# Kernel tuning notes

Hardware: AMD Instinct MI355X
Metric: run time of the kernel (lower is better)

The kernel has to match this reference:

```python
import jax, jax.numpy as jnp
import numpy as np

B, L, H = 32, 512, 1024
Q = 128
VA_H = 256

def setup_inputs() -> dict:
    key = jax.random.key(0)
    ks = jax.random.split(key, 12)
    hidden_states = jax.random.normal(ks[0], (B, L, H), dtype=jnp.float32)
    # Build valid inclusive spans: start in [2, L-16), length in [0, 8)
    asp_s = jax.random.randint(ks[1], (B, Q), 2, L - 16)
    asp_e = asp_s + jax.random.randint(ks[2], (B, Q), 0, 8)
    opi_s = jax.random.randint(ks[3], (B, Q), 2, L - 16)
    opi_e = opi_s + jax.random.randint(ks[4], (B, Q), 0, 8)
    null = jax.random.uniform(ks[5], (B, Q)) < 0.1
    asp_s = jnp.where(null, 0, asp_s)
    quad_spans = jnp.stack([asp_s, asp_e, opi_s, opi_e], axis=-1).astype(jnp.int64)
    quad_mask = (jax.random.uniform(ks[6], (B, Q)) > 0.3).astype(jnp.float32)
    # MLP params (torch Linear: y = x @ W.T + b), kaiming-ish scale
    def lin(k, out_d, in_d):
        return jax.random.normal(k, (out_d, in_d), dtype=jnp.float32) / np.sqrt(in_d)
    W1 = lin(ks[7], VA_H, 3 * H); b1 = jnp.zeros((VA_H,), jnp.float32)
    W2 = lin(ks[8], VA_H // 2, VA_H); b2 = jnp.zeros((VA_H // 2,), jnp.float32)
    W3 = lin(ks[9], 2, VA_H // 2); b3 = jnp.zeros((2,), jnp.float32)
    return {"hidden_states": hidden_states, "quad_spans": quad_spans,
            "quad_mask": quad_mask, "W1": W1, "b1": b1, "W2": W2, "b2": b2,
            "W3": W3, "b3": b3}

def _pool_spans(hidden_states, s, e):
    # hidden_states: [B,L,H]; s,e: [B,Q] inclusive indices
    pos = jnp.arange(hidden_states.shape[1])  # [L]
    valid = (s >= 2) & (e >= s)               # [B,Q]
    m = (pos[None, None, :] >= s[..., None]) & (pos[None, None, :] <= e[..., None])
    m = (m & valid[..., None]).astype(hidden_states.dtype)  # [B,Q,L]
    cnt = jnp.maximum(m.sum(-1, keepdims=True), 1.0)        # [B,Q,1]
    mean = jnp.einsum('bql,blh->bqh', m, hidden_states) / cnt
    sep = hidden_states[:, 1:2, :]                           # [B,1,H] fallback
    return jnp.where(valid[..., None], mean, sep)

def reference(hidden_states, quad_spans, quad_mask, W1, b1, W2, b2, W3, b3):
    h_asp = _pool_spans(hidden_states, quad_spans[..., 0], quad_spans[..., 1])
    h_opi = _pool_spans(hidden_states, quad_spans[..., 2], quad_spans[..., 3])
    h_pair = jnp.concatenate([h_asp, h_opi, h_asp * h_opi], axis=-1)  # [B,Q,3H]
    x = jax.nn.gelu(h_pair @ W1.T + b1, approximate=False)  # torch GELU = erf
    x = jax.nn.gelu(x @ W2.T + b2, approximate=False)
    va = jax.nn.sigmoid(x @ W3.T + b3) * 8.0 + 1.0          # [B,Q,2] in [1,9]
    # Invalid pairs stay zero, matching the torch loop's skipped entries
    return va * (quad_mask >= 0.5).astype(va.dtype)[..., None]
```

## Files before the change

kernel.cpp:

```cpp
#include <hip/hip_runtime.h>
#include <hip/hip_bf16.h>
#include <math.h>

typedef __bf16 bf16x8 __attribute__((ext_vector_type(8)));
typedef float f32x4 __attribute__((ext_vector_type(4)));

__device__ __forceinline__ unsigned short f2bf(float x) {
    union { float f; unsigned int u; } v; v.f = x;
    unsigned int r = v.u + 0x7fffu + ((v.u >> 16) & 1u);
    return (unsigned short)(r >> 16);
}
__device__ __forceinline__ float gelu_exact(float v) {
    return 0.5f * v * (1.0f + erff(v * 0.70710678118654752f));
}

__global__ __launch_bounds__(256) void prep_kernel(const float* __restrict__ hs,
                                                   const int* __restrict__ spans,
                                                   const float* __restrict__ W1,
                                                   unsigned short* __restrict__ hp,
                                                   unsigned short* __restrict__ w1b,
                                                   float* __restrict__ xacc1) {
    const int blk = blockIdx.x;
    const int tid = threadIdx.x;

    if (blk >= 4096) {
        if (blk < 4864) {
            const int i = (blk - 4096) * 256 + tid;
            float4 f = ((const float4*)W1)[i];
            ushort4 u;
            u.x = f2bf(f.x); u.y = f2bf(f.y); u.z = f2bf(f.z); u.w = f2bf(f.w);
            ((ushort4*)w1b)[i] = u;
        } else {
            const int i = (blk - 4864) * 256 + tid;
            ((float4*)xacc1)[i] = make_float4(0.f, 0.f, 0.f, 0.f);
        }
        return;
    }

    const int pair = blk;
    const int b = pair >> 7;

    const bool is64 = (spans[1] == 0);
    int s_a, e_a, s_o, e_o;
    if (is64) {
        s_a = spans[(pair * 4 + 0) * 2]; e_a = spans[(pair * 4 + 1) * 2];
        s_o = spans[(pair * 4 + 2) * 2]; e_o = spans[(pair * 4 + 3) * 2];
    } else {
        s_a = spans[pair * 4 + 0]; e_a = spans[pair * 4 + 1];
        s_o = spans[pair * 4 + 2]; e_o = spans[pair * 4 + 3];
    }

    const float4* base = (const float4*)hs + (size_t)b * 512 * 256;

    float4 A, O;
    if (s_a >= 2 && e_a >= s_a) {
        float sx = 0.f, sy = 0.f, sz = 0.f, sw = 0.f;
        for (int t = s_a; t <= e_a; ++t) {
            float4 v = base[t * 256 + tid];
            sx += v.x; sy += v.y; sz += v.z; sw += v.w;
        }
        float inv = 1.0f / (float)(e_a - s_a + 1);
        A.x = sx * inv; A.y = sy * inv; A.z = sz * inv; A.w = sw * inv;
    } else {
        A = base[256 + tid];
    }
    if (s_o >= 2 && e_o >= s_o) {
        float sx = 0.f, sy = 0.f, sz = 0.f, sw = 0.f;
        for (int t = s_o; t <= e_o; ++t) {
            float4 v = base[t * 256 + tid];
            sx += v.x; sy += v.y; sz += v.z; sw += v.w;
        }
        float inv = 1.0f / (float)(e_o - s_o + 1);
        O.x = sx * inv; O.y = sy * inv; O.z = sz * inv; O.w = sw * inv;
    } else {
        O = base[256 + tid];
    }

    unsigned short* row = hp + (size_t)pair * 3072;
    const int d = tid * 4;
    ushort4 pa, po, pp;
    pa.x = f2bf(A.x); pa.y = f2bf(A.y); pa.z = f2bf(A.z); pa.w = f2bf(A.w);
    po.x = f2bf(O.x); po.y = f2bf(O.y); po.z = f2bf(O.z); po.w = f2bf(O.w);
    pp.x = f2bf(A.x * O.x); pp.y = f2bf(A.y * O.y);
    pp.z = f2bf(A.z * O.z); pp.w = f2bf(A.w * O.w);
    *(ushort4*)(row + d) = pa;
    *(ushort4*)(row + 1024 + d) = po;
    *(ushort4*)(row + 2048 + d) = pp;
}

__global__ __launch_bounds__(256, 2) void gemm1_mfma(const unsigned short* __restrict__ A,
                                                     const unsigned short* __restrict__ Bw,
                                                     float* __restrict__ xacc) {
    __shared__ __align__(16) unsigned short As[128 * 64];
    __shared__ __align__(16) unsigned short Bs[128 * 64];

    const int tid = threadIdx.x;
    const int lane = tid & 63;
    const int wid = tid >> 6;
    const int quad = lane >> 4;
    const int l16 = lane & 15;
    const int wM = (wid >> 1) * 64;
    const int wN = (wid & 1) * 64;
    const int m0 = blockIdx.x * 128;
    const int n0 = blockIdx.y * 128;
    const int kb = blockIdx.z * 384;

    const int srow = tid >> 3;
    const int lchunk = (tid & 7) ^ (srow & 7);
    const unsigned short* Abase = A + (size_t)(m0 + srow) * 3072 + kb + lchunk * 8;
    const unsigned short* Bbase = Bw + (size_t)(n0 + srow) * 3072 + kb + lchunk * 8;

    int aoff[4][2], boff[4][2];
#pragma unroll
    for (int mi = 0; mi < 4; ++mi) {
#pragma unroll
        for (int h = 0; h < 2; ++h) {
            int row = wM + mi * 16 + l16;
            int pc = (h * 4 + quad) ^ (row & 7);
            aoff[mi][h] = row * 64 + pc * 8;
            row = wN + mi * 16 + l16;
            pc = (h * 4 + quad) ^ (row & 7);
            boff[mi][h] = row * 64 + pc * 8;
        }
    }

    f32x4 acc[4][4] = {};

#pragma unroll
    for (int it = 0; it < 6; ++it) {
        const int kadv = it * 64;
#pragma unroll
        for (int j = 0; j < 4; ++j) {
            __builtin_amdgcn_global_load_lds(
                (const __attribute__((address_space(1))) void*)(Abase + (size_t)j * 32 * 3072 + kadv),
                (__attribute__((address_space(3))) void*)(&As[(j * 256 + tid) * 8]),
                16, 0, 0);
            __builtin_amdgcn_global_load_lds(
                (const __attribute__((address_space(1))) void*)(Bbase + (size_t)j * 32 * 3072 + kadv),
                (__attribute__((address_space(3))) void*)(&Bs[(j * 256 + tid) * 8]),
                16, 0, 0);
        }
        __syncthreads();
#pragma unroll
        for (int h = 0; h < 2; ++h) {
            bf16x8 af[4], bfr[4];
#pragma unroll
            for (int mi = 0; mi < 4; ++mi) af[mi] = *(const bf16x8*)&As[aoff[mi][h]];
#pragma unroll
            for (int ni = 0; ni < 4; ++ni) bfr[ni] = *(const bf16x8*)&Bs[boff[ni][h]];
#pragma unroll
            for (int mi = 0; mi < 4; ++mi)
#pragma unroll
                for (int ni = 0; ni < 4; ++ni)
                    acc[mi][ni] = __builtin_amdgcn_mfma_f32_16x16x32_bf16(
                        af[mi], bfr[ni], acc[mi][ni], 0, 0, 0);
        }
        __syncthreads();
    }

#pragma unroll
    for (int mi = 0; mi < 4; ++mi) {
#pragma unroll
        for (int ni = 0; ni < 4; ++ni) {
            const int n = n0 + wN + ni * 16 + l16;
#pragma unroll
            for (int rr = 0; rr < 4; ++rr) {
                const int m = m0 + wM + mi * 16 + quad * 4 + rr;
                unsafeAtomicAdd(&xacc[(size_t)m * 256 + n], acc[mi][ni][rr]);
            }
        }
    }
}

__global__ __launch_bounds__(256) void gelu_bias(const float* __restrict__ xacc,
                                                 const float* __restrict__ bias,
                                                 unsigned short* __restrict__ xout,
                                                 int total4, int ncols4) {
    for (int i = blockIdx.x * blockDim.x + threadIdx.x; i < total4;
         i += gridDim.x * blockDim.x) {
        float4 v = ((const float4*)xacc)[i];
        float4 bv = ((const float4*)bias)[i & (ncols4 - 1)];
        ushort4 u;
        u.x = f2bf(gelu_exact(v.x + bv.x));
        u.y = f2bf(gelu_exact(v.y + bv.y));
        u.z = f2bf(gelu_exact(v.z + bv.z));
        u.w = f2bf(gelu_exact(v.w + bv.w));
        ((ushort4*)xout)[i] = u;
    }
}

__global__ __launch_bounds__(256) void mlp2_head(const unsigned short* __restrict__ x1,
                                                 const float* __restrict__ W2f,
                                                 const float* __restrict__ b2,
                                                 const float* __restrict__ W3,
                                                 const float* __restrict__ b3,
                                                 const float* __restrict__ mask,
                                                 float* __restrict__ out) {
    __shared__ __align__(16) unsigned short Xs[32][72];
    __shared__ __align__(16) unsigned short Ws[128][72];
    __shared__ float X2[32][132];

    const int tid = threadIdx.x;
    const int lane = tid & 63;
    const int wid = tid >> 6;
    const int wM = (wid >> 1) * 16;
    const int wN = (wid & 1) * 64;
    const int quad = lane >> 4;
    const int l16 = lane & 15;
    const int m0 = blockIdx.x * 32;

    f32x4 acc[4] = {};

    for (int k0 = 0; k0 < 256; k0 += 64) {
        {
            const int r = tid >> 3, c = (tid & 7) * 8;
            *(uint4*)&Xs[r][c] = *(const uint4*)(x1 + (size_t)(m0 + r) * 256 + k0 + c);
        }
#pragma unroll
        for (int p = 0; p < 4; ++p) {
            const int v = tid + p * 256;
            const int r = v >> 3, c = (v & 7) * 8;
            const float* src = W2f + (size_t)r * 256 + k0 + c;
            float4 f0 = *(const float4*)src;
            float4 f1 = *(const float4*)(src + 4);
            ushort4 u;
            u.x = f2bf(f0.x); u.y = f2bf(f0.y); u.z = f2bf(f0.z); u.w = f2bf(f0.w);
            *(ushort4*)&Ws[r][c] = u;
            u.x = f2bf(f1.x); u.y = f2bf(f1.y); u.z = f2bf(f1.z); u.w = f2bf(f1.w);
            *(ushort4*)&Ws[r][c + 4] = u;
        }
        __syncthreads();
#pragma unroll
        for (int kk = 0; kk < 64; kk += 32) {
            bf16x8 a = *(const bf16x8*)&Xs[wM + l16][kk + quad * 8];
#pragma unroll
            for (int ni = 0; ni < 4; ++ni) {
                bf16x8 b = *(const bf16x8*)&Ws[wN + ni * 16 + l16][kk + quad * 8];
                acc[ni] = __builtin_amdgcn_mfma_f32_16x16x32_bf16(a, b, acc[ni], 0, 0, 0);
            }
        }
        __syncthreads();
    }

#pragma unroll
    for (int ni = 0; ni < 4; ++ni) {
        const int n = wN + ni * 16 + l16;
        const float bn = b2[n];
#pragma unroll
        for (int rr = 0; rr < 4; ++rr) {
            const int m = wM + quad * 4 + rr;
            X2[m][n] = gelu_exact(acc[ni][rr] + bn);
        }
    }
    __syncthreads();

    const int p = tid >> 3;
    const int cc = (tid & 7) * 16;
    float a0 = 0.f, a1 = 0.f;
#pragma unroll
    for (int j = 0; j < 16; ++j) {
        const float xv = X2[p][cc + j];
        a0 += xv * W3[cc + j];
        a1 += xv * W3[128 + cc + j];
    }
    a0 += __shfl_xor(a0, 1); a0 += __shfl_xor(a0, 2); a0 += __shfl_xor(a0, 4);
    a1 += __shfl_xor(a1, 1); a1 += __shfl_xor(a1, 2); a1 += __shfl_xor(a1, 4);
    if ((tid & 7) == 0) {
        const int pair = m0 + p;
        const float mk = (mask[pair] >= 0.5f) ? 1.0f : 0.0f;
        out[pair * 2 + 0] = ((1.0f / (1.0f + expf(-(a0 + b3[0])))) * 8.0f + 1.0f) * mk;
        out[pair * 2 + 1] = ((1.0f / (1.0f + expf(-(a1 + b3[1])))) * 8.0f + 1.0f) * mk;
    }
}

extern "C" void kernel_launch(void* const* d_in, const int* in_sizes, int n_in,
                              void* d_out, int out_size, void* d_ws, size_t ws_size,
                              hipStream_t stream) {
    const float* hs   = (const float*)d_in[0];
    const int*   spans= (const int*)d_in[1];
    const float* mask = (const float*)d_in[2];
    const float* W1   = (const float*)d_in[3];
    const float* b1   = (const float*)d_in[4];
    const float* W2   = (const float*)d_in[5];
    const float* b2   = (const float*)d_in[6];
    const float* W3   = (const float*)d_in[7];
    const float* b3   = (const float*)d_in[8];
    float* out = (float*)d_out;

    unsigned short* hp    = (unsigned short*)d_ws;
    float*          xacc1 = (float*)((char*)d_ws + 25165824);
    unsigned short* w1b   = (unsigned short*)((char*)d_ws + 29360128);
    unsigned short* x1    = (unsigned short*)d_ws;

    prep_kernel<<<dim3(5888), dim3(256), 0, stream>>>(hs, spans, W1, hp, w1b, xacc1);
    gemm1_mfma<<<dim3(32, 2, 8), dim3(256), 0, stream>>>(hp, w1b, xacc1);
    gelu_bias<<<dim3(512), dim3(256), 0, stream>>>(xacc1, b1, x1, 4096 * 256 / 4, 64);
    mlp2_head<<<dim3(128), dim3(256), 0, stream>>>(x1, W2, b2, W3, b3, mask, out);
}
```

Before: 166.4 us.

## Fuse GELU, second MLP layer and head into GEMM1 via last-block counter

The separate gelu_bias and mlp2_head kernels are removed. Each GEMM1 block increments a per-row-tile atomic counter after its split-K atomic adds, and the 16th (last) block for a 128-row tile reads the accumulated fp32 results, applies bias and GELU, and runs the 256->128 MLP with MFMA plus the 2-output head. This saves two kernel launches and the bf16 intermediate round-trip, at the cost of serialising the tail work onto 32 last-arriving blocks. It also relies on correct fences and atomics for cross-block visibility.

```diff
diff --git a/kernel.cpp b/kernel.cpp
--- a/kernel.cpp
+++ b/kernel.cpp
@@ -9,6 +9,10 @@
     union { float f; unsigned int u; } v; v.f = x;
     unsigned int r = v.u + 0x7fffu + ((v.u >> 16) & 1u);
     return (unsigned short)(r >> 16);
+}
+__device__ __forceinline__ float bf2f(unsigned short h) {
+    union { unsigned int u; float f; } v; v.u = ((unsigned int)h) << 16;
+    return v.f;
 }
 __device__ __forceinline__ float gelu_exact(float v) {
     return 0.5f * v * (1.0f + erff(v * 0.70710678118654752f));
@@ -19,12 +23,14 @@
                                                    const float* __restrict__ W1,
                                                    unsigned short* __restrict__ hp,
                                                    unsigned short* __restrict__ w1b,
-                                                   float* __restrict__ xacc1) {
+                                                   float* __restrict__ xacc1,
+                                                   int* __restrict__ cnt) {
     const int blk = blockIdx.x;
     const int tid = threadIdx.x;
 
     if (blk >= 4096) {
         if (blk < 4864) {
+            if (blk == 4096 && tid < 32) cnt[tid] = 0;
             const int i = (blk - 4096) * 256 + tid;
             float4 f = ((const float4*)W1)[i];
             ushort4 u;
@@ -88,11 +94,21 @@
     *(ushort4*)(row + 2048 + d) = pp;
 }
 
-__global__ __launch_bounds__(256, 2) void gemm1_mfma(const unsigned short* __restrict__ A,
+__global__ __launch_bounds__(256, 2) void gemm_fused(const unsigned short* __restrict__ A,
                                                      const unsigned short* __restrict__ Bw,
-                                                     float* __restrict__ xacc) {
-    __shared__ __align__(16) unsigned short As[128 * 64];
-    __shared__ __align__(16) unsigned short Bs[128 * 64];
+                                                     float* __restrict__ xacc,
+                                                     const float* __restrict__ b1,
+                                                     const float* __restrict__ W2f,
+                                                     const float* __restrict__ b2,
+                                                     const float* __restrict__ W3,
+                                                     const float* __restrict__ b3,
+                                                     const float* __restrict__ mask,
+                                                     float* __restrict__ out,
+                                                     int* __restrict__ cnt) {
+    __shared__ __align__(16) unsigned short smem[17408];
+    __shared__ int s_last;
+    unsigned short* As = smem;
+    unsigned short* Bs = smem + 8192;
 
     const int tid = threadIdx.x;
     const int lane = tid & 63;
@@ -124,21 +140,98 @@
         }
     }
 
-    f32x4 acc[4][4] = {};
-
-#pragma unroll
-    for (int it = 0; it < 6; ++it) {
-        const int kadv = it * 64;
-#pragma unroll
-        for (int j = 0; j < 4; ++j) {
-            __builtin_amdgcn_global_load_lds(
-                (const __attribute__((address_space(1))) void*)(Abase + (size_t)j * 32 * 3072 + kadv),
-                (__attribute__((address_space(3))) void*)(&As[(j * 256 + tid) * 8]),
-                16, 0, 0);
-            __builtin_amdgcn_global_load_lds(
-                (const __attribute__((address_space(1))) void*)(Bbase + (size_t)j * 32 * 3072 + kadv),
-                (__attribute__((address_space(3))) void*)(&Bs[(j * 256 + tid) * 8]),
-                16, 0, 0);
+    {
+        f32x4 acc[4][4] = {};
+#pragma unroll
+        for (int it = 0; it < 6; ++it) {
+            const int kadv = it * 64;
+#pragma unroll
+            for (int j = 0; j < 4; ++j) {
+                __builtin_amdgcn_global_load_lds(
+                    (const __attribute__((address_space(1))) void*)(Abase + (size_t)j * 32 * 3072 + kadv),
+                    (__attribute__((address_space(3))) void*)(&As[(j * 256 + tid) * 8]),
+                    16, 0, 0);
+                __builtin_amdgcn_global_load_lds(
+                    (const __attribute__((address_space(1))) void*)(Bbase + (size_t)j * 32 * 3072 + kadv),
+                    (__attribute__((address_space(3))) void*)(&Bs[(j * 256 + tid) * 8]),
+                    16, 0, 0);
+            }
+            __syncthreads();
+#pragma unroll
+            for (int h = 0; h < 2; ++h) {
+                bf16x8 af[4], bfr[4];
+#pragma unroll
+                for (int mi = 0; mi < 4; ++mi) af[mi] = *(const bf16x8*)&As[aoff[mi][h]];
+#pragma unroll
+                for (int ni = 0; ni < 4; ++ni) bfr[ni] = *(const bf16x8*)&Bs[boff[ni][h]];
+#pragma unroll
+                for (int mi = 0; mi < 4; ++mi)
+#pragma unroll
+                    for (int ni = 0; ni < 4; ++ni)
+                        acc[mi][ni] = __builtin_amdgcn_mfma_f32_16x16x32_bf16(
+                            af[mi], bfr[ni], acc[mi][ni], 0, 0, 0);
+            }
+            __syncthreads();
+        }
+
+#pragma unroll
+        for (int mi = 0; mi < 4; ++mi) {
+#pragma unroll
+            for (int ni = 0; ni < 4; ++ni) {
+                const int n = n0 + wN + ni * 16 + l16;
+#pragma unroll
+                for (int rr = 0; rr < 4; ++rr) {
+                    const int m = m0 + wM + mi * 16 + quad * 4 + rr;
+                    unsafeAtomicAdd(&xacc[(size_t)m * 256 + n], acc[mi][ni][rr]);
+                }
+            }
+        }
+    }
+
+    __syncthreads();
+    if (tid == 0) {
+        __threadfence();
+        int old = __hip_atomic_fetch_add(&cnt[blockIdx.x], 1,
+                                         __ATOMIC_ACQ_REL, __HIP_MEMORY_SCOPE_AGENT);
+        s_last = (old == 15) ? 1 : 0;
+    }
+    __syncthreads();
+    if (!s_last) return;
+
+    f32x4 acc2[4][4] = {};
+#pragma unroll
+    for (int kc = 0; kc < 4; ++kc) {
+#pragma unroll
+        for (int s4 = 0; s4 < 4; ++s4) {
+            const int s = s4 * 256 + tid;
+            const int row = s >> 3;
+            const int pc = s & 7;
+            const int lc = pc ^ (row & 7);
+            const int col = kc * 64 + lc * 8;
+            const float* xsrc = xacc + (size_t)(m0 + row) * 256 + col;
+            float v[8];
+#pragma unroll
+            for (int j = 0; j < 8; ++j)
+                v[j] = __hip_atomic_load(xsrc + j, __ATOMIC_RELAXED,
+                                         __HIP_MEMORY_SCOPE_AGENT);
+            ushort4 u0, u1;
+            u0.x = f2bf(gelu_exact(v[0] + b1[col + 0]));
+            u0.y = f2bf(gelu_exact(v[1] + b1[col + 1]));
+            u0.z = f2bf(gelu_exact(v[2] + b1[col + 2]));
+            u0.w = f2bf(gelu_exact(v[3] + b1[col + 3]));
+            u1.x = f2bf(gelu_exact(v[4] + b1[col + 4]));
+            u1.y = f2bf(gelu_exact(v[5] + b1[col + 5]));
+            u1.z = f2bf(gelu_exact(v[6] + b1[col + 6]));
+            u1.w = f2bf(gelu_exact(v[7] + b1[col + 7]));
+            *(ushort4*)&As[s * 8] = u0;
+            *(ushort4*)&As[s * 8 + 4] = u1;
+            const float* wsrc = W2f + (size_t)row * 256 + col;
+            float4 f0 = *(const float4*)wsrc;
+            float4 f1 = *(const float4*)(wsrc + 4);
+            u0.x = f2bf(f0.x); u0.y = f2bf(f0.y); u0.z = f2bf(f0.z); u0.w = f2bf(f0.w);
+            u1.x = f2bf(f1.x); u1.y = f2bf(f1.y); u1.z = f2bf(f1.z); u1.w = f2bf(f1.w);
+            *(ushort4*)&Bs[s * 8] = u0;
+            *(ushort4*)&Bs[s * 8 + 4] = u1;
         }
         __syncthreads();
 #pragma unroll
@@ -152,8 +245,8 @@
             for (int mi = 0; mi < 4; ++mi)
 #pragma unroll
                 for (int ni = 0; ni < 4; ++ni)
-                    acc[mi][ni] = __builtin_amdgcn_mfma_f32_16x16x32_bf16(
-                        af[mi], bfr[ni], acc[mi][ni], 0, 0, 0);
+                    acc2[mi][ni] = __builtin_amdgcn_mfma_f32_16x16x32_bf16(
+                        af[mi], bfr[ni], acc2[mi][ni], 0, 0, 0);
         }
         __syncthreads();
     }
@@ -162,110 +255,29 @@
     for (int mi = 0; mi < 4; ++mi) {
 #pragma unroll
         for (int ni = 0; ni < 4; ++ni) {
-            const int n = n0 + wN + ni * 16 + l16;
+            const int col = wN + ni * 16 + l16;
+            const float bn = b2[col];
 #pragma unroll
             for (int rr = 0; rr < 4; ++rr) {
-                const int m = m0 + wM + mi * 16 + quad * 4 + rr;
-                unsafeAtomicAdd(&xacc[(size_t)m * 256 + n], acc[mi][ni][rr]);
+                const int row = wM + mi * 16 + quad * 4 + rr;
+                smem[row * 136 + col] = f2bf(gelu_exact(acc2[mi][ni][rr] + bn));
             }
         }
     }
-}
-
-__global__ __launch_bounds__(256) void gelu_bias(const float* __restrict__ xacc,
-                                                 const float* __restrict__ bias,
-                                                 unsigned short* __restrict__ xout,
-                                                 int total4, int ncols4) {
-    for (int i = blockIdx.x * blockDim.x + threadIdx.x; i < total4;
-         i += gridDim.x * blockDim.x) {
-        float4 v = ((const float4*)xacc)[i];
-        float4 bv = ((const float4*)bias)[i & (ncols4 - 1)];
-        ushort4 u;
-        u.x = f2bf(gelu_exact(v.x + bv.x));
-        u.y = f2bf(gelu_exact(v.y + bv.y));
-        u.z = f2bf(gelu_exact(v.z + bv.z));
-        u.w = f2bf(gelu_exact(v.w + bv.w));
-        ((ushort4*)xout)[i] = u;
-    }
-}
-
-__global__ __launch_bounds__(256) void mlp2_head(const unsigned short* __restrict__ x1,
-                                                 const float* __restrict__ W2f,
-                                                 const float* __restrict__ b2,
-                                                 const float* __restrict__ W3,
-                                                 const float* __restrict__ b3,
-                                                 const float* __restrict__ mask,
-                                                 float* __restrict__ out) {
-    __shared__ __align__(16) unsigned short Xs[32][72];
-    __shared__ __align__(16) unsigned short Ws[128][72];
-    __shared__ float X2[32][132];
-
-    const int tid = threadIdx.x;
-    const int lane = tid & 63;
-    const int wid = tid >> 6;
-    const int wM = (wid >> 1) * 16;
-    const int wN = (wid & 1) * 64;
-    const int quad = lane >> 4;
-    const int l16 = lane & 15;
-    const int m0 = blockIdx.x * 32;
-
-    f32x4 acc[4] = {};
-
-    for (int k0 = 0; k0 < 256; k0 += 64) {
-        {
-            const int r = tid >> 3, c = (tid & 7) * 8;
-            *(uint4*)&Xs[r][c] = *(const uint4*)(x1 + (size_t)(m0 + r) * 256 + k0 + c);
-        }
-#pragma unroll
-        for (int p = 0; p < 4; ++p) {
-            const int v = tid + p * 256;
-            const int r = v >> 3, c = (v & 7) * 8;
-            const float* src = W2f + (size_t)r * 256 + k0 + c;
-            float4 f0 = *(const float4*)src;
-            float4 f1 = *(const float4*)(src + 4);
-            ushort4 u;
-            u.x = f2bf(f0.x); u.y = f2bf(f0.y); u.z = f2bf(f0.z); u.w = f2bf(f0.w);
-            *(ushort4*)&Ws[r][c] = u;
-            u.x = f2bf(f1.x); u.y = f2bf(f1.y); u.z = f2bf(f1.z); u.w = f2bf(f1.w);
-            *(ushort4*)&Ws[r][c + 4] = u;
-        }
-        __syncthreads();
-#pragma unroll
-        for (int kk = 0; kk < 64; kk += 32) {
-            bf16x8 a = *(const bf16x8*)&Xs[wM + l16][kk + quad * 8];
-#pragma unroll
-            for (int ni = 0; ni < 4; ++ni) {
-                bf16x8 b = *(const bf16x8*)&Ws[wN + ni * 16 + l16][kk + quad * 8];
-                acc[ni] = __builtin_amdgcn_mfma_f32_16x16x32_bf16(a, b, acc[ni], 0, 0, 0);
-            }
-        }
-        __syncthreads();
-    }
-
-#pragma unroll
-    for (int ni = 0; ni < 4; ++ni) {
-        const int n = wN + ni * 16 + l16;
-        const float bn = b2[n];
-#pragma unroll
-        for (int rr = 0; rr < 4; ++rr) {
-            const int m = wM + quad * 4 + rr;
-            X2[m][n] = gelu_exact(acc[ni][rr] + bn);
-        }
-    }
     __syncthreads();
 
-    const int p = tid >> 3;
-    const int cc = (tid & 7) * 16;
+    const int p = tid >> 1;
+    const int half = (tid & 1) * 64;
     float a0 = 0.f, a1 = 0.f;
 #pragma unroll
-    for (int j = 0; j < 16; ++j) {
-        const float xv = X2[p][cc + j];
-        a0 += xv * W3[cc + j];
-        a1 += xv * W3[128 + cc + j];
-    }
-    a0 += __shfl_xor(a0, 1); a0 += __shfl_xor(a0, 2); a0 += __shfl_xor(a0, 4);
-    a1 += __shfl_xor(a1, 1); a1 += __shfl_xor(a1, 2); a1 += __shfl_xor(a1, 4);
-    if ((tid & 7) == 0) {
+    for (int j = 0; j < 64; ++j) {
+        const float xv = bf2f(smem[p * 136 + half + j]);
+        a0 += xv * W3[half + j];
+        a1 += xv * W3[128 + half + j];
+    }
+    a0 += __shfl_xor(a0, 1);
+    a1 += __shfl_xor(a1, 1);
+    if ((tid & 1) == 0) {
         const int pair = m0 + p;
         const float mk = (mask[pair] >= 0.5f) ? 1.0f : 0.0f;
         out[pair * 2 + 0] = ((1.0f / (1.0f + expf(-(a0 + b3[0])))) * 8.0f + 1.0f) * mk;
@@ -290,10 +302,9 @@
     unsigned short* hp    = (unsigned short*)d_ws;
     float*          xacc1 = (float*)((char*)d_ws + 25165824);
     unsigned short* w1b   = (unsigned short*)((char*)d_ws + 29360128);
-    unsigned short* x1    = (unsigned short*)d_ws;
-
-    prep_kernel<<<dim3(5888), dim3(256), 0, stream>>>(hs, spans, W1, hp, w1b, xacc1);
-    gemm1_mfma<<<dim3(32, 2, 8), dim3(256), 0, stream>>>(hp, w1b, xacc1);
-    gelu_bias<<<dim3(512), dim3(256), 0, stream>>>(xacc1, b1, x1, 4096 * 256 / 4, 64);
-    mlp2_head<<<dim3(128), dim3(256), 0, stream>>>(x1, W2, b2, W3, b3, mask, out);
-}
+    int*            cnt   = (int*)((char*)d_ws + 30932992);
+
+    prep_kernel<<<dim3(5888), dim3(256), 0, stream>>>(hs, spans, W1, hp, w1b, xacc1, cnt);
+    gemm_fused<<<dim3(32, 2, 8), dim3(256), 0, stream>>>(hp, w1b, xacc1, b1, W2, b2,
+                                                         W3, b3, mask, out, cnt);
+}
```

Result: slower. 205.2 us (+23.4%).

## Fuse bias+GELU into MLP2 head and retile GEMM1 to 128x64 blocks

Applied to the files above, without the earlier changes.

Removes the standalone gelu_bias kernel. The MLP2 head now reads the fp32 split-K accumulator directly and applies bias, exact GELU and bf16 conversion while staging into shared memory, which saves one launch and a round trip of the intermediate. GEMM1 output tiles shrink from 128x128 to 128x64, doubling the grid to 1024 blocks. Each wave accumulates a 32x64 sub-tile with half the accumulators, and launch bounds rise to 4 blocks per CU. The tradeoff is more A-tile reloads per output element and lower MFMA work per LDS load.

```diff
diff --git a/kernel.cpp b/kernel.cpp
--- a/kernel.cpp
+++ b/kernel.cpp
@@ -88,21 +88,20 @@
     *(ushort4*)(row + 2048 + d) = pp;
 }
 
-__global__ __launch_bounds__(256, 2) void gemm1_mfma(const unsigned short* __restrict__ A,
+__global__ __launch_bounds__(256, 4) void gemm1_mfma(const unsigned short* __restrict__ A,
                                                      const unsigned short* __restrict__ Bw,
                                                      float* __restrict__ xacc) {
     __shared__ __align__(16) unsigned short As[128 * 64];
-    __shared__ __align__(16) unsigned short Bs[128 * 64];
+    __shared__ __align__(16) unsigned short Bs[64 * 64];
 
     const int tid = threadIdx.x;
     const int lane = tid & 63;
     const int wid = tid >> 6;
     const int quad = lane >> 4;
     const int l16 = lane & 15;
-    const int wM = (wid >> 1) * 64;
-    const int wN = (wid & 1) * 64;
+    const int wM = wid * 32;
     const int m0 = blockIdx.x * 128;
-    const int n0 = blockIdx.y * 128;
+    const int n0 = blockIdx.y * 64;
     const int kb = blockIdx.z * 384;
 
     const int srow = tid >> 3;
@@ -110,21 +109,24 @@
     const unsigned short* Abase = A + (size_t)(m0 + srow) * 3072 + kb + lchunk * 8;
     const unsigned short* Bbase = Bw + (size_t)(n0 + srow) * 3072 + kb + lchunk * 8;
 
-    int aoff[4][2], boff[4][2];
-#pragma unroll
-    for (int mi = 0; mi < 4; ++mi) {
-#pragma unroll
-        for (int h = 0; h < 2; ++h) {
-            int row = wM + mi * 16 + l16;
-            int pc = (h * 4 + quad) ^ (row & 7);
+    int aoff[2][2], boff[4][2];
+#pragma unroll
+    for (int h = 0; h < 2; ++h) {
+#pragma unroll
+        for (int mi = 0; mi < 2; ++mi) {
+            const int row = wM + mi * 16 + l16;
+            const int pc = (h * 4 + quad) ^ (row & 7);
             aoff[mi][h] = row * 64 + pc * 8;
-            row = wN + mi * 16 + l16;
-            pc = (h * 4 + quad) ^ (row & 7);
-            boff[mi][h] = row * 64 + pc * 8;
-        }
-    }
-
-    f32x4 acc[4][4] = {};
+        }
+#pragma unroll
+        for (int ni = 0; ni < 4; ++ni) {
+            const int row = ni * 16 + l16;
+            const int pc = (h * 4 + quad) ^ (row & 7);
+            boff[ni][h] = row * 64 + pc * 8;
+        }
+    }
+
+    f32x4 acc[2][4] = {};
 
 #pragma unroll
     for (int it = 0; it < 6; ++it) {
@@ -135,6 +137,9 @@
                 (const __attribute__((address_space(1))) void*)(Abase + (size_t)j * 32 * 3072 + kadv),
                 (__attribute__((address_space(3))) void*)(&As[(j * 256 + tid) * 8]),
                 16, 0, 0);
+        }
+#pragma unroll
+        for (int j = 0; j < 2; ++j) {
             __builtin_amdgcn_global_load_lds(
                 (const __attribute__((address_space(1))) void*)(Bbase + (size_t)j * 32 * 3072 + kadv),
                 (__attribute__((address_space(3))) void*)(&Bs[(j * 256 + tid) * 8]),
@@ -143,13 +148,13 @@
         __syncthreads();
 #pragma unroll
         for (int h = 0; h < 2; ++h) {
-            bf16x8 af[4], bfr[4];
-#pragma unroll
-            for (int mi = 0; mi < 4; ++mi) af[mi] = *(const bf16x8*)&As[aoff[mi][h]];
+            bf16x8 af[2], bfr[4];
+#pragma unroll
+            for (int mi = 0; mi < 2; ++mi) af[mi] = *(const bf16x8*)&As[aoff[mi][h]];
 #pragma unroll
             for (int ni = 0; ni < 4; ++ni) bfr[ni] = *(const bf16x8*)&Bs[boff[ni][h]];
 #pragma unroll
-            for (int mi = 0; mi < 4; ++mi)
+            for (int mi = 0; mi < 2; ++mi)
 #pragma unroll
                 for (int ni = 0; ni < 4; ++ni)
                     acc[mi][ni] = __builtin_amdgcn_mfma_f32_16x16x32_bf16(
@@ -159,10 +164,10 @@
     }
 
 #pragma unroll
-    for (int mi = 0; mi < 4; ++mi) {
+    for (int mi = 0; mi < 2; ++mi) {
 #pragma unroll
         for (int ni = 0; ni < 4; ++ni) {
-            const int n = n0 + wN + ni * 16 + l16;
+            const int n = n0 + ni * 16 + l16;
 #pragma unroll
             for (int rr = 0; rr < 4; ++rr) {
                 const int m = m0 + wM + mi * 16 + quad * 4 + rr;
@@ -172,30 +177,14 @@
     }
 }
 
-__global__ __launch_bounds__(256) void gelu_bias(const float* __restrict__ xacc,
-                                                 const float* __restrict__ bias,
-                                                 unsigned short* __restrict__ xout,
-                                                 int total4, int ncols4) {
-    for (int i = blockIdx.x * blockDim.x + threadIdx.x; i < total4;
-         i += gridDim.x * blockDim.x) {
-        float4 v = ((const float4*)xacc)[i];
-        float4 bv = ((const float4*)bias)[i & (ncols4 - 1)];
-        ushort4 u;
-        u.x = f2bf(gelu_exact(v.x + bv.x));
-        u.y = f2bf(gelu_exact(v.y + bv.y));
-        u.z = f2bf(gelu_exact(v.z + bv.z));
-        u.w = f2bf(gelu_exact(v.w + bv.w));
-        ((ushort4*)xout)[i] = u;
-    }
-}
-
-__global__ __launch_bounds__(256) void mlp2_head(const unsigned short* __restrict__ x1,
-                                                 const float* __restrict__ W2f,
-                                                 const float* __restrict__ b2,
-                                                 const float* __restrict__ W3,
-                                                 const float* __restrict__ b3,
-                                                 const float* __restrict__ mask,
-                                                 float* __restrict__ out) {
+__global__ __launch_bounds__(256) void mlp2g_head(const float* __restrict__ xacc,
+                                                  const float* __restrict__ b1,
+                                                  const float* __restrict__ W2f,
+                                                  const float* __restrict__ b2,
+                                                  const float* __restrict__ W3,
+                                                  const float* __restrict__ b3,
+                                                  const float* __restrict__ mask,
+                                                  float* __restrict__ out) {
     __shared__ __align__(16) unsigned short Xs[32][72];
     __shared__ __align__(16) unsigned short Ws[128][72];
     __shared__ float X2[32][132];
@@ -214,7 +203,18 @@
     for (int k0 = 0; k0 < 256; k0 += 64) {
         {
             const int r = tid >> 3, c = (tid & 7) * 8;
-            *(uint4*)&Xs[r][c] = *(const uint4*)(x1 + (size_t)(m0 + r) * 256 + k0 + c);
+            const float* src = xacc + (size_t)(m0 + r) * 256 + k0 + c;
+            float4 f0 = *(const float4*)src;
+            float4 f1 = *(const float4*)(src + 4);
+            float4 g0 = *(const float4*)(b1 + k0 + c);
+            float4 g1 = *(const float4*)(b1 + k0 + c + 4);
+            ushort4 u0, u1;
+            u0.x = f2bf(gelu_exact(f0.x + g0.x)); u0.y = f2bf(gelu_exact(f0.y + g0.y));
+            u0.z = f2bf(gelu_exact(f0.z + g0.z)); u0.w = f2bf(gelu_exact(f0.w + g0.w));
+            u1.x = f2bf(gelu_exact(f1.x + g1.x)); u1.y = f2bf(gelu_exact(f1.y + g1.y));
+            u1.z = f2bf(gelu_exact(f1.z + g1.z)); u1.w = f2bf(gelu_exact(f1.w + g1.w));
+            *(ushort4*)&Xs[r][c] = u0;
+            *(ushort4*)&Xs[r][c + 4] = u1;
         }
 #pragma unroll
         for (int p = 0; p < 4; ++p) {
@@ -290,10 +290,8 @@
     unsigned short* hp    = (unsigned short*)d_ws;
     float*          xacc1 = (float*)((char*)d_ws + 25165824);
     unsigned short* w1b   = (unsigned short*)((char*)d_ws + 29360128);
-    unsigned short* x1    = (unsigned short*)d_ws;
 
     prep_kernel<<<dim3(5888), dim3(256), 0, stream>>>(hs, spans, W1, hp, w1b, xacc1);
-    gemm1_mfma<<<dim3(32, 2, 8), dim3(256), 0, stream>>>(hp, w1b, xacc1);
-    gelu_bias<<<dim3(512), dim3(256), 0, stream>>>(xacc1, b1, x1, 4096 * 256 / 4, 64);
-    mlp2_head<<<dim3(128), dim3(256), 0, stream>>>(x1, W2, b2, W3, b3, mask, out);
-}
+    gemm1_mfma<<<dim3(32, 4, 8), dim3(256), 0, stream>>>(hp, w1b, xacc1);
+    mlp2g_head<<<dim3(128), dim3(256), 0, stream>>>(xacc1, b1, W2, b2, W3, b3, mask, out);
+}
```

New measurement: 161.3 us. 1.03x faster.

## Replace split-K atomic GEMM with full-K double-buffered GEMM fused with bias+GELU

Applied to the files above, without the earlier changes.

The first-layer GEMM no longer splits K across blocks with float atomics into a zeroed accumulator. Each block now computes a 16x64 output tile over the full K=3072 with double-buffered LDS loads, then applies bias and exact GELU in the epilogue and writes bf16 directly. This removes the accumulator zeroing, the atomic traffic and the separate gelu_bias launch. In exchange the tiles are much smaller, so the hidden-pair operand is reloaded once per N-tile and each wave does only one MFMA per half-step, which lowers arithmetic intensity and data reuse.

```diff
diff --git a/kernel.cpp b/kernel.cpp
--- a/kernel.cpp
+++ b/kernel.cpp
@@ -18,22 +18,16 @@
                                                    const int* __restrict__ spans,
                                                    const float* __restrict__ W1,
                                                    unsigned short* __restrict__ hp,
-                                                   unsigned short* __restrict__ w1b,
-                                                   float* __restrict__ xacc1) {
+                                                   unsigned short* __restrict__ w1b) {
     const int blk = blockIdx.x;
     const int tid = threadIdx.x;
 
     if (blk >= 4096) {
-        if (blk < 4864) {
-            const int i = (blk - 4096) * 256 + tid;
-            float4 f = ((const float4*)W1)[i];
-            ushort4 u;
-            u.x = f2bf(f.x); u.y = f2bf(f.y); u.z = f2bf(f.z); u.w = f2bf(f.w);
-            ((ushort4*)w1b)[i] = u;
-        } else {
-            const int i = (blk - 4864) * 256 + tid;
-            ((float4*)xacc1)[i] = make_float4(0.f, 0.f, 0.f, 0.f);
-        }
+        const int i = (blk - 4096) * 256 + tid;
+        float4 f = ((const float4*)W1)[i];
+        ushort4 u;
+        u.x = f2bf(f.x); u.y = f2bf(f.y); u.z = f2bf(f.z); u.w = f2bf(f.w);
+        ((ushort4*)w1b)[i] = u;
         return;
     }
 
@@ -88,104 +82,78 @@
     *(ushort4*)(row + 2048 + d) = pp;
 }
 
-__global__ __launch_bounds__(256, 2) void gemm1_mfma(const unsigned short* __restrict__ A,
+__global__ __launch_bounds__(256, 8) void gemm1_gelu(const unsigned short* __restrict__ A,
                                                      const unsigned short* __restrict__ Bw,
-                                                     float* __restrict__ xacc) {
-    __shared__ __align__(16) unsigned short As[128 * 64];
-    __shared__ __align__(16) unsigned short Bs[128 * 64];
+                                                     const float* __restrict__ b1,
+                                                     unsigned short* __restrict__ x1) {
+    __shared__ __align__(16) unsigned short As[2][16 * 64];
+    __shared__ __align__(16) unsigned short Bs[2][64 * 64];
 
     const int tid = threadIdx.x;
     const int lane = tid & 63;
     const int wid = tid >> 6;
     const int quad = lane >> 4;
     const int l16 = lane & 15;
-    const int wM = (wid >> 1) * 64;
-    const int wN = (wid & 1) * 64;
-    const int m0 = blockIdx.x * 128;
-    const int n0 = blockIdx.y * 128;
-    const int kb = blockIdx.z * 384;
+    const int m0 = blockIdx.x * 16;
+    const int n0 = blockIdx.y * 64;
 
     const int srow = tid >> 3;
-    const int lchunk = (tid & 7) ^ (srow & 7);
-    const unsigned short* Abase = A + (size_t)(m0 + srow) * 3072 + kb + lchunk * 8;
-    const unsigned short* Bbase = Bw + (size_t)(n0 + srow) * 3072 + kb + lchunk * 8;
-
-    int aoff[4][2], boff[4][2];
-#pragma unroll
-    for (int mi = 0; mi < 4; ++mi) {
+    const int lch = (tid & 7) ^ (srow & 7);
+    const unsigned short* Aptr = A + (size_t)(m0 + srow) * 3072 + lch * 8;
+    const unsigned short* Bptr = Bw + (size_t)(n0 + srow) * 3072 + lch * 8;
+
+    int aoff[2], boff[2];
+#pragma unroll
+    for (int h = 0; h < 2; ++h) {
+        int pc = (h * 4 + quad) ^ (l16 & 7);
+        aoff[h] = l16 * 64 + pc * 8;
+        const int brow = wid * 16 + l16;
+        pc = (h * 4 + quad) ^ (brow & 7);
+        boff[h] = brow * 64 + pc * 8;
+    }
+
+    f32x4 acc = {};
+
+    if (tid < 128)
+        __builtin_amdgcn_global_load_lds(
+            (const __attribute__((address_space(1))) void*)Aptr,
+            (__attribute__((address_space(3))) void*)(&As[0][tid * 8]), 16, 0, 0);
+#pragma unroll
+    for (int j = 0; j < 2; ++j)
+        __builtin_amdgcn_global_load_lds(
+            (const __attribute__((address_space(1))) void*)(Bptr + (size_t)j * 32 * 3072),
+            (__attribute__((address_space(3))) void*)(&Bs[0][(j * 256 + tid) * 8]), 16, 0, 0);
+
+    for (int it = 0; it < 48; ++it) {
+        const int cur = it & 1;
+        __syncthreads();
+        if (it + 1 < 48) {
+            const int nxt = cur ^ 1;
+            const int kadv = (it + 1) * 64;
+            if (tid < 128)
+                __builtin_amdgcn_global_load_lds(
+                    (const __attribute__((address_space(1))) void*)(Aptr + kadv),
+                    (__attribute__((address_space(3))) void*)(&As[nxt][tid * 8]), 16, 0, 0);
+#pragma unroll
+            for (int j = 0; j < 2; ++j)
+                __builtin_amdgcn_global_load_lds(
+                    (const __attribute__((address_space(1))) void*)(Bptr + (size_t)j * 32 * 3072 + kadv),
+                    (__attribute__((address_space(3))) void*)(&Bs[nxt][(j * 256 + tid) * 8]), 16, 0, 0);
+        }
 #pragma unroll
         for (int h = 0; h < 2; ++h) {
-            int row = wM + mi * 16 + l16;
-            int pc = (h * 4 + quad) ^ (row & 7);
-            aoff[mi][h] = row * 64 + pc * 8;
-            row = wN + mi * 16 + l16;
-            pc = (h * 4 + quad) ^ (row & 7);
-            boff[mi][h] = row * 64 + pc * 8;
-        }
-    }
-
-    f32x4 acc[4][4] = {};
-
-#pragma unroll
-    for (int it = 0; it < 6; ++it) {
-        const int kadv = it * 64;
-#pragma unroll
-        for (int j = 0; j < 4; ++j) {
-            __builtin_amdgcn_global_load_lds(
-                (const __attribute__((address_space(1))) void*)(Abase + (size_t)j * 32 * 3072 + kadv),
-                (__attribute__((address_space(3))) void*)(&As[(j * 256 + tid) * 8]),
-                16, 0, 0);
-            __builtin_amdgcn_global_load_lds(
-                (const __attribute__((address_space(1))) void*)(Bbase + (size_t)j * 32 * 3072 + kadv),
-                (__attribute__((address_space(3))) void*)(&Bs[(j * 256 + tid) * 8]),
-                16, 0, 0);
-        }
-        __syncthreads();
-#pragma unroll
-        for (int h = 0; h < 2; ++h) {
-            bf16x8 af[4], bfr[4];
-#pragma unroll
-            for (int mi = 0; mi < 4; ++mi) af[mi] = *(const bf16x8*)&As[aoff[mi][h]];
-#pragma unroll
-            for (int ni = 0; ni < 4; ++ni) bfr[ni] = *(const bf16x8*)&Bs[boff[ni][h]];
-#pragma unroll
-            for (int mi = 0; mi < 4; ++mi)
-#pragma unroll
-                for (int ni = 0; ni < 4; ++ni)
-                    acc[mi][ni] = __builtin_amdgcn_mfma_f32_16x16x32_bf16(
-                        af[mi], bfr[ni], acc[mi][ni], 0, 0, 0);
-        }
-        __syncthreads();
-    }
-
-#pragma unroll
-    for (int mi = 0; mi < 4; ++mi) {
-#pragma unroll
-        for (int ni = 0; ni < 4; ++ni) {
-            const int n = n0 + wN + ni * 16 + l16;
-#pragma unroll
-            for (int rr = 0; rr < 4; ++rr) {
-                const int m = m0 + wM + mi * 16 + quad * 4 + rr;
-                unsafeAtomicAdd(&xacc[(size_t)m * 256 + n], acc[mi][ni][rr]);
-            }
-        }
-    }
-}
-
-__global__ __launch_bounds__(256) void gelu_bias(const float* __restrict__ xacc,
-                                                 const float* __restrict__ bias,
-                                                 unsigned short* __restrict__ xout,
-                                                 int total4, int ncols4) {
-    for (int i = blockIdx.x * blockDim.x + threadIdx.x; i < total4;
-         i += gridDim.x * blockDim.x) {
-        float4 v = ((const float4*)xacc)[i];
-        float4 bv = ((const float4*)bias)[i & (ncols4 - 1)];
-        ushort4 u;
-        u.x = f2bf(gelu_exact(v.x + bv.x));
-        u.y = f2bf(gelu_exact(v.y + bv.y));
-        u.z = f2bf(gelu_exact(v.z + bv.z));
-        u.w = f2bf(gelu_exact(v.w + bv.w));
-        ((ushort4*)xout)[i] = u;
+            bf16x8 a = *(const bf16x8*)&As[cur][aoff[h]];
+            bf16x8 b = *(const bf16x8*)&Bs[cur][boff[h]];
+            acc = __builtin_amdgcn_mfma_f32_16x16x32_bf16(a, b, acc, 0, 0, 0);
+        }
+    }
+
+    const int n = n0 + wid * 16 + l16;
+    const float bn = b1[n];
+#pragma unroll
+    for (int rr = 0; rr < 4; ++rr) {
+        const int m = m0 + quad * 4 + rr;
+        x1[(size_t)m * 256 + n] = f2bf(gelu_exact(acc[rr] + bn));
     }
 }
 
@@ -287,13 +255,11 @@
     const float* b3   = (const float*)d_in[8];
     float* out = (float*)d_out;
 
-    unsigned short* hp    = (unsigned short*)d_ws;
-    float*          xacc1 = (float*)((char*)d_ws + 25165824);
-    unsigned short* w1b   = (unsigned short*)((char*)d_ws + 29360128);
-    unsigned short* x1    = (unsigned short*)d_ws;
-
-    prep_kernel<<<dim3(5888), dim3(256), 0, stream>>>(hs, spans, W1, hp, w1b, xacc1);
-    gemm1_mfma<<<dim3(32, 2, 8), dim3(256), 0, stream>>>(hp, w1b, xacc1);
-    gelu_bias<<<dim3(512), dim3(256), 0, stream>>>(xacc1, b1, x1, 4096 * 256 / 4, 64);
+    unsigned short* hp  = (unsigned short*)d_ws;
+    unsigned short* w1b = (unsigned short*)((char*)d_ws + 25165824);
+    unsigned short* x1  = (unsigned short*)((char*)d_ws + 26738688);
+
+    prep_kernel<<<dim3(4864), dim3(256), 0, stream>>>(hs, spans, W1, hp, w1b);
+    gemm1_gelu<<<dim3(256, 4), dim3(256), 0, stream>>>(hp, w1b, b1, x1);
     mlp2_head<<<dim3(128), dim3(256), 0, stream>>>(x1, W2, b2, W3, b3, mask, out);
 }
```

After: 157.2 us. -5.5%, faster.
